# Kernel optimization log

Measured on AMD Instinct MI355X. Metric: run time of the kernel, lower is better.

The kernel has to match this reference:

```python
import jax, jax.numpy as jnp
import numpy as np

N = 50000      # nodes
E = 800000     # edges
FEAT = 128     # input feature dim
EMB = 256      # embed_dim = heads * hid
H = 4          # attention heads
C = 64         # hid_dim per head
PED = 32       # positional encoding dim
NEG_SLOPE = 0.2


def setup_inputs() -> dict:
    key = jax.random.key(0)
    ks = jax.random.split(key, 20)
    s = lambda i, shape, sc=0.1: jax.random.normal(ks[i], shape, jnp.float32) * sc
    return {
        "x": s(0, (N, FEAT), 1.0),
        "x_masked": s(1, (N, FEAT), 1.0),
        "PE": s(2, (N, PED), 1.0),
        "PE_noise": s(3, (N, PED), 1.0),
        "edge_index": jax.random.randint(ks[4], (2, E), 0, N),
        # PEG positional encoder (linear + relu)
        "W_peg": s(5, (PED, PED)), "b_peg": jnp.zeros((PED,), jnp.float32),
        # GAT layer 0
        "W0": s(6, (FEAT, H * C)), "a_s0": s(7, (H, C)), "a_d0": s(8, (H, C)),
        "w_pe0": s(9, (H,)), "W_u0": s(10, (PED, PED)),
        # GAT layer 1
        "W1": s(11, (EMB, H * C)), "a_s1": s(12, (H, C)), "a_d1": s(13, (H, C)),
        "w_pe1": s(14, (H,)), "W_u1": s(15, (PED, PED)),
    }


def _gat(x, pe, src, dst, W, a_s, a_d, w_pe, W_u):
    # PE-aware GATConv: standard GAT attention + PE-distance bias per head.
    xp = (x @ W).reshape(-1, H, C)                       # [N,H,C]
    al_s = (xp * a_s).sum(-1)                            # [N,H]
    al_d = (xp * a_d).sum(-1)                            # [N,H]
    dist = jnp.sqrt(((pe[src] - pe[dst]) ** 2).sum(-1) + 1e-8)   # [E]
    logits = jax.nn.leaky_relu(al_s[src] + al_d[dst], NEG_SLOPE) \
             + dist[:, None] * w_pe                      # [E,H]
    # segment softmax over incoming edges of each dst node
    m = jax.ops.segment_max(logits, dst, num_segments=N)
    e = jnp.exp(logits - m[dst])
    den = jax.ops.segment_sum(e, dst, num_segments=N)
    alpha = e / (den[dst] + 1e-16)                       # [E,H]
    out = jax.ops.segment_sum(alpha[:, :, None] * xp[src], dst,
                              num_segments=N).reshape(-1, H * C)  # [N,H*C]
    pe_out = jax.nn.relu(pe @ W_u)                       # per-layer PE update
    return out, pe_out


def reference(x, x_masked, PE, PE_noise, W_peg, b_peg,
              W0, a_s0, a_d0, w_pe0, W_u0,
              W1, a_s1, a_d1, w_pe1, W_u1, edge_index):
    src, dst = edge_index[0], edge_index[1]
    # PEG encoder on both PE branches
    pe = jax.nn.relu(PE @ W_peg + b_peg)
    pe_n = jax.nn.relu(PE_noise @ W_peg + b_peg)
    # layer 0 (dual branches; eval mode -> dropout is identity)
    h, pe_n = _gat(x, pe_n, src, dst, W0, a_s0, a_d0, w_pe0, W_u0)
    hm, pe = _gat(x_masked, pe, src, dst, W0, a_s0, a_d0, w_pe0, W_u0)
    h = jax.nn.relu(h)
    hm = jax.nn.relu(hm)
    # layer 1 (last layer: no activation)
    h, pe_n = _gat(h, pe_n, src, dst, W1, a_s1, a_d1, w_pe1, W_u1)
    hm, pe = _gat(hm, pe, src, dst, W1, a_s1, a_d1, w_pe1, W_u1)
    return (hm, pe_n)
```

## Files before the change

kernel.cpp:

```cpp
#include <hip/hip_runtime.h>
#include <hip/hip_bf16.h>

#define N_NODES 50000
#define N_EDGES 800000
#define NEG_SLOPE 0.2f

typedef __hip_bfloat16 bf16;
typedef __attribute__((ext_vector_type(8))) short short8;
typedef __attribute__((ext_vector_type(4))) float f32x4;
typedef __attribute__((ext_vector_type(2))) float f32x2;

__device__ __forceinline__ float b2f(bf16 x) { return __bfloat162float(x); }

__device__ __forceinline__ float ldsel(const void* p, size_t i, int isbf) {
  return isbf ? __bfloat162float(((const bf16*)p)[i]) : ((const float*)p)[i];
}
__device__ __forceinline__ void stsel(void* p, size_t i, int isbf, float v) {
  if (isbf) ((bf16*)p)[i] = __float2bfloat16(v);
  else ((float*)p)[i] = v;
}

__device__ __forceinline__ int block_detect(const unsigned short* __restrict__ probe) {
  __shared__ int wcount;
  int tid = threadIdx.x;
  if (tid == 0) wcount = 0;
  __syncthreads();
  int ex = (probe[2 * tid] >> 7) & 0xFF;
  unsigned long long m = __ballot(ex >= 0x85);
  if ((tid & 63) == 0) atomicAdd(&wcount, __popcll(m));
  __syncthreads();
  return wcount < 8;
}

struct CvtJobs {
  const void* src[10];
  float* dst[10];
  int n[10];
};
__global__ __launch_bounds__(256) void prep_kernel(CvtJobs jobs,
                                                   const unsigned short* __restrict__ probe,
                                                   const void* __restrict__ W0in,
                                                   bf16* __restrict__ Wt0,
                                                   const void* __restrict__ W1in,
                                                   bf16* __restrict__ Wt1,
                                                   int* __restrict__ flag,
                                                   const int* __restrict__ dst,
                                                   int* __restrict__ deg) {
  int tid = threadIdx.x;
  int b = blockIdx.x;
  if (b >= 400) {
    int e = (b - 400) * 256 + tid;
    atomicAdd(&deg[dst[e]], 1);
    return;
  }
  int isbf = block_detect(probe);
  if (b == 0 && tid == 0) *flag = isbf;
  if (b < 16) {
    for (int j = 0; j < 10; j++) {
      int n = jobs.n[j];
      const void* s = jobs.src[j];
      float* d = jobs.dst[j];
      for (int i = b * 256 + tid; i < n; i += 16 * 256) d[i] = ldsel(s, i, isbf);
    }
  } else if (b < 16 + 128) {
    int i = (b - 16) * 256 + tid;
    int n = i >> 7, k = i & 127;
    Wt0[i] = __float2bfloat16(ldsel(W0in, (size_t)k * 256 + n, isbf));
  } else {
    int i = (b - 144) * 256 + tid;
    int n = i >> 8, k = i & 255;
    Wt1[i] = __float2bfloat16(ldsel(W1in, (size_t)k * 256 + n, isbf));
  }
}

__global__ __launch_bounds__(1024) void scan_kernel(const int* __restrict__ deg,
                                                    int* __restrict__ rowptr,
                                                    int* __restrict__ bsum,
                                                    int* __restrict__ flags, int n) {
  __shared__ int wsum[16];
  __shared__ int spre;
  int tid = threadIdx.x;
  int idx = blockIdx.x * 1024 + tid;
  int v = (idx < n) ? deg[idx] : 0;
  int incl = v;
#pragma unroll
  for (int off = 1; off < 64; off <<= 1) {
    int t = __shfl_up(incl, off);
    if ((tid & 63) >= off) incl += t;
  }
  int wid = tid >> 6;
  if ((tid & 63) == 63) wsum[wid] = incl;
  __syncthreads();
  if (tid == 0) {
    int acc = 0;
#pragma unroll
    for (int w = 0; w < 16; w++) {
      int t = wsum[w];
      wsum[w] = acc;
      acc += t;
    }
    atomicExch(&bsum[blockIdx.x], acc);
    if (atomicAdd(&flags[0], 1) == 48) {
      int a = 0;
      for (int j = 0; j < 49; j++) {
        int t = atomicAdd(&bsum[j], 0);
        atomicExch(&bsum[j], a);
        a += t;
      }
      atomicExch(&flags[1], 1);
    }
    while (atomicAdd(&flags[1], 0) == 0) {}
    spre = atomicAdd(&bsum[blockIdx.x], 0);
  }
  __syncthreads();
  if (idx < n) rowptr[idx + 1] = spre + wsum[wid] + incl;
  if (idx == 0) rowptr[0] = 0;
}

template <int K, bool A_DUAL>
__device__ __forceinline__ void gemm_body(char* smem, int bid, int tid,
                                          const void* __restrict__ Ap,
                                          const bf16* __restrict__ Bt,
                                          bf16* __restrict__ C, int M,
                                          const float* __restrict__ a_sf,
                                          const float* __restrict__ a_df,
                                          char* __restrict__ blob,
                                          float* __restrict__ al_d,
                                          const int* __restrict__ flag) {
  constexpr int LDK = 72;
  short* a_lds = (short*)smem;
  short* b_lds = (short*)(smem + 64 * LDK * 2);
  float* lds_al = (float*)(smem + 2 * 64 * LDK * 2);
  int nrt = (M + 63) / 64;
  int xcd = bid & 7;
  int jj = bid >> 3;
  int col_t = jj & 3;
  int row_t = (jj >> 2) * 8 + xcd;
  if (row_t >= nrt) return;
  int isbf = A_DUAL ? *flag : 1;
  int row0 = row_t * 64;
  int col0 = col_t * 64;
  int lane = tid & 63;
  int wv = tid >> 6;
  int wm = (wv & 1) * 32, wn = (wv >> 1) * 32;
  int l15 = lane & 15, quad = lane >> 4;
  if (tid < 128) lds_al[tid] = 0.f;
  f32x4 acc00 = {0.f, 0.f, 0.f, 0.f}, acc01 = acc00, acc10 = acc00, acc11 = acc00;

  for (int kb = 0; kb < K; kb += 64) {
    if (kb) __syncthreads();
    for (int idx = tid; idx < 64 * 8; idx += 256) {
      int r = idx >> 3, sidx = idx & 7;
      int gr = row0 + r;
      size_t gi = (size_t)gr * K + kb + sidx * 8;
      uint4 av = make_uint4(0u, 0u, 0u, 0u);
      if (A_DUAL && !isbf) {
        if (gr < M) {
          float4 f0 = ((const float4*)Ap)[gi / 4];
          float4 f1 = ((const float4*)Ap)[gi / 4 + 1];
          union { uint4 v; bf16 h[8]; } o;
          o.h[0] = __float2bfloat16(f0.x);
          o.h[1] = __float2bfloat16(f0.y);
          o.h[2] = __float2bfloat16(f0.z);
          o.h[3] = __float2bfloat16(f0.w);
          o.h[4] = __float2bfloat16(f1.x);
          o.h[5] = __float2bfloat16(f1.y);
          o.h[6] = __float2bfloat16(f1.z);
          o.h[7] = __float2bfloat16(f1.w);
          av = o.v;
        }
      } else {
        if (gr < M) av = *(const uint4*)&((const bf16*)Ap)[gi];
      }
      *(uint4*)&a_lds[r * LDK + sidx * 8] = av;
      *(uint4*)&b_lds[r * LDK + sidx * 8] =
          *(const uint4*)&Bt[(size_t)(col0 + r) * K + kb + sidx * 8];
    }
    __syncthreads();
#pragma unroll
    for (int k0 = 0; k0 < 64; k0 += 32) {
      int ko = k0 + quad * 8;
      short8 a0 = *(const short8*)&a_lds[(wm + l15) * LDK + ko];
      short8 a1 = *(const short8*)&a_lds[(wm + 16 + l15) * LDK + ko];
      short8 b0 = *(const short8*)&b_lds[(wn + l15) * LDK + ko];
      short8 b1 = *(const short8*)&b_lds[(wn + 16 + l15) * LDK + ko];
      acc00 = __builtin_amdgcn_mfma_f32_16x16x32_bf16(a0, b0, acc00, 0, 0, 0);
      acc01 = __builtin_amdgcn_mfma_f32_16x16x32_bf16(a0, b1, acc01, 0, 0, 0);
      acc10 = __builtin_amdgcn_mfma_f32_16x16x32_bf16(a1, b0, acc10, 0, 0, 0);
      acc11 = __builtin_amdgcn_mfma_f32_16x16x32_bf16(a1, b1, acc11, 0, 0, 0);
    }
  }
  const f32x4* accs[2][2] = {{&acc00, &acc01}, {&acc10, &acc11}};
  float as0 = a_sf[col0 + wn + l15], as1 = a_sf[col0 + wn + 16 + l15];
  float ad0 = a_df[col0 + wn + l15], ad1 = a_df[col0 + wn + 16 + l15];
#pragma unroll
  for (int i = 0; i < 2; i++) {
    float sp[4], dp[4];
#pragma unroll
    for (int r = 0; r < 4; r++) {
      float v0 = (*accs[i][0])[r], v1 = (*accs[i][1])[r];
      sp[r] = v0 * as0 + v1 * as1;
      dp[r] = v0 * ad0 + v1 * ad1;
      int grow = row0 + wm + i * 16 + quad * 4 + r;
      if (grow < M) {
        C[(size_t)grow * 256 + col0 + wn + l15] = __float2bfloat16(v0);
        C[(size_t)grow * 256 + col0 + wn + 16 + l15] = __float2bfloat16(v1);
      }
    }
#pragma unroll
    for (int off = 1; off < 16; off <<= 1) {
#pragma unroll
      for (int r = 0; r < 4; r++) {
        sp[r] += __shfl_xor(sp[r], off);
        dp[r] += __shfl_xor(dp[r], off);
      }
    }
    if (l15 == 0) {
#pragma unroll
      for (int r = 0; r < 4; r++) {
        int lrow = wm + i * 16 + quad * 4 + r;
        atomicAdd(&lds_al[lrow], sp[r]);
        atomicAdd(&lds_al[64 + lrow], dp[r]);
      }
    }
  }
  __syncthreads();
  if (tid < 64 && row0 + tid < M) {
    int row = row0 + tid;
    *(float*)(blob + (size_t)row * 128 + 64 + (size_t)col_t * 4) = lds_al[tid];
    al_d[(size_t)row * 4 + col_t] = lds_al[64 + tid];
  }
}

#define SMEM_BYTES (2 * 64 * 72 * 2 + 512)

template <int K, bool A_DUAL>
__global__ __launch_bounds__(256) void mfma_gemm(const void* __restrict__ Ap,
                                                 const bf16* __restrict__ Bt,
                                                 bf16* __restrict__ C, int M,
                                                 const float* __restrict__ a_sf,
                                                 const float* __restrict__ a_df,
                                                 char* __restrict__ blob,
                                                 float* __restrict__ al_d,
                                                 const int* __restrict__ flag) {
  __shared__ char smem[SMEM_BYTES];
  gemm_body<K, A_DUAL>(smem, blockIdx.x, threadIdx.x, Ap, Bt, C, M, a_sf, a_df,
                       blob, al_d, flag);
}

#define NGEMM0 3136
#define NCHUNK (N_EDGES / 256)
#define NFILL8 (NCHUNK * 8)
#define NDIV8 (N_NODES / 8)
__global__ __launch_bounds__(256) void mid_kernel(const void* __restrict__ Ap,
                                                  const bf16* __restrict__ Wt0,
                                                  bf16* __restrict__ xp,
                                                  const float* __restrict__ a_s0,
                                                  const float* __restrict__ a_d0,
                                                  float* __restrict__ al_d,
                                                  const int* __restrict__ src,
                                                  const int* __restrict__ dst,
                                                  const int* __restrict__ rowptr,
                                                  int* __restrict__ fill,
                                                  int* __restrict__ csr_src,
                                                  const void* __restrict__ pen,
                                                  const void* __restrict__ pem,
                                                  const float* __restrict__ Wpeg,
                                                  const float* __restrict__ bpeg,
                                                  const float* __restrict__ Wu0,
                                                  const float* __restrict__ Wu1,
                                                  void* out, size_t out_off,
                                                  char* __restrict__ blob0,
                                                  char* __restrict__ blob1,
                                                  const int* __restrict__ flag) {
  __shared__ char smem[SMEM_BYTES];
  int tid = threadIdx.x;
  int b = blockIdx.x;
  if (b < NGEMM0) {
    gemm_body<128, true>(smem, b, tid, Ap, Wt0, xp, N_NODES, a_s0, a_d0, blob0,
                         al_d, flag);
    return;
  }
  b -= NGEMM0;
  if (b < NFILL8) {
    int xcd = b & 7;
    int e = (b >> 3) * 256 + tid;
    int d = dst[e];
    int lo = xcd * NDIV8;
    if (d >= lo && d < lo + NDIV8) {
      int pos = atomicAdd(&fill[d], 1);
      csr_src[rowptr[d] + pos] = src[e];
    }
    return;
  }
  int pb = b - NFILL8;
  float* w1 = (float*)smem;
  float* w2 = w1 + 1024;
  float* w3 = w2 + 1024;
  float* rowA = w3 + 1024;
  float* rowB = rowA + 256;
  int isbf = *flag;
  bool c3 = pb < NDIV8;
  int n0 = (c3 ? pb : pb - NDIV8) * 8;
  const void* in = c3 ? pen : pem;
  for (int i = tid; i < 1024; i += 256) {
    w1[i] = Wpeg[i];
    w2[i] = Wu0[i];
    if (c3) w3[i] = Wu1[i];
  }
  rowA[tid] = ldsel(in, (size_t)n0 * 32 + tid, isbf);
  __syncthreads();
  int col = tid & 31, ln = tid >> 5;
  size_t bi = ((size_t)(n0 + ln)) * 64 + col;
  float acc = bpeg[col];
#pragma unroll
  for (int j = 0; j < 32; j++) acc += rowA[ln * 32 + j] * w1[j * 32 + col];
  acc = fmaxf(acc, 0.f);
  if (!c3) ((bf16*)blob0)[bi] = __float2bfloat16(acc);
  rowB[tid] = acc;
  __syncthreads();
  acc = 0.f;
#pragma unroll
  for (int j = 0; j < 32; j++) acc += rowB[ln * 32 + j] * w2[j * 32 + col];
  acc = fmaxf(acc, 0.f);
  if (!c3) {
    ((bf16*)blob1)[bi] = __float2bfloat16(acc);
    return;
  }
  rowA[tid] = acc;
  __syncthreads();
  acc = 0.f;
#pragma unroll
  for (int j = 0; j < 32; j++) acc += rowA[ln * 32 + j] * w3[j * 32 + col];
  stsel(out, out_off + (size_t)n0 * 32 + tid, isbf, fmaxf(acc, 0.f));
}

template <bool RELU, bool OUT_DUAL>
__global__ __launch_bounds__(256) void agg_kernel(const bf16* __restrict__ xp,
                                                  const char* __restrict__ blob,
                                                  const float* __restrict__ al_d,
                                                  const float* __restrict__ w_pe,
                                                  const int* __restrict__ csr_src,
                                                  const int* __restrict__ rowptr,
                                                  void* out, const int* __restrict__ flag) {
  int isbf = OUT_DUAL ? *flag : 1;
  int lane = threadIdx.x & 63;
  int n = blockIdx.x * 4 + (threadIdx.x >> 6);
  int q = lane >> 4, li = lane & 15, h = li >> 2;
  const char* bn = blob + (size_t)n * 128;
  unsigned int ud = *(const unsigned int*)(bn + li * 4);
  float pdlo = __uint_as_float(ud << 16);
  float pdhi = __uint_as_float(ud & 0xffff0000u);
  float ald = al_d[(size_t)n * 4 + h];
  float wph = w_pe[h];
  int s1 = rowptr[n + 1];
  int s = rowptr[n] + q;
  f32x2 acc2[8];
#pragma unroll
  for (int j = 0; j < 8; j++) acc2[j] = (f32x2){0.f, 0.f};
  float asum = 0.f;

  int sn_c = -1, sn_n = -1;
  unsigned int pes_c = 0, pes_n = 0;
  float als_c = 0.f, als_n = 0.f;
  uint4 z = make_uint4(0u, 0u, 0u, 0u);
  uint4 xc0 = z, xc1 = z, xn0 = z, xn1 = z;
  if (s < s1) {
    sn_c = csr_src[s];
    const char* bs = blob + (size_t)sn_c * 128;
    pes_c = *(const unsigned int*)(bs + li * 4);
    als_c = *(const float*)(bs + 64 + h * 4);
    const uint4* b = (const uint4*)&xp[(size_t)sn_c * 256 + li * 16];
    xc0 = b[0];
    xc1 = b[1];
    if (s + 4 < s1) sn_n = csr_src[s + 4];
  }
  int sf = s + 8;
  while (sn_c >= 0) {
    if (sn_n >= 0) {
      const char* bs = blob + (size_t)sn_n * 128;
      pes_n = *(const unsigned int*)(bs + li * 4);
      als_n = *(const float*)(bs + 64 + h * 4);
      const uint4* b = (const uint4*)&xp[(size_t)sn_n * 256 + li * 16];
      xn0 = b[0];
      xn1 = b[1];
    }
    int sn_f = (sf < s1) ? csr_src[sf] : -1;
    sf += 4;
    float dx = __uint_as_float(pes_c << 16) - pdlo;
    float dy = __uint_as_float(pes_c & 0xffff0000u) - pdhi;
    float d2 = dx * dx + dy * dy;
#pragma unroll
    for (int off = 1; off < 16; off <<= 1) d2 += __shfl_xor(d2, off);
    float lg = als_c + ald;
    lg = fmaxf(lg, 0.f) + NEG_SLOPE * fminf(lg, 0.f);
    lg += __builtin_amdgcn_sqrtf(d2 + 1e-8f) * wph;
    float a = __expf(lg);
    f32x2 av = {a, a};
    unsigned int u[8] = {xc0.x, xc0.y, xc0.z, xc0.w, xc1.x, xc1.y, xc1.z, xc1.w};
#pragma unroll
    for (int p = 0; p < 8; p++) {
      f32x2 xv;
      xv.x = __uint_as_float(u[p] << 16);
      xv.y = __uint_as_float(u[p] & 0xffff0000u);
      acc2[p] += av * xv;
    }
    asum += a;
    sn_c = sn_n;
    pes_c = pes_n;
    als_c = als_n;
    xc0 = xn0;
    xc1 = xn1;
    sn_n = sn_f;
  }
#pragma unroll
  for (int j = 0; j < 8; j++) {
    acc2[j].x += __shfl_xor(acc2[j].x, 16);
    acc2[j].x += __shfl_xor(acc2[j].x, 32);
    acc2[j].y += __shfl_xor(acc2[j].y, 16);
    acc2[j].y += __shfl_xor(acc2[j].y, 32);
  }
  asum += __shfl_xor(asum, 16);
  asum += __shfl_xor(asum, 32);
  if (q == 0) {
    float inv = 1.f / (asum + 1e-16f);
    size_t oi = (size_t)n * 256 + li * 16;
    if (OUT_DUAL && !isbf) {
      float* of = (float*)out;
#pragma unroll
      for (int p = 0; p < 4; p++) {
        float4 f;
        f.x = acc2[2 * p].x * inv;
        f.y = acc2[2 * p].y * inv;
        f.z = acc2[2 * p + 1].x * inv;
        f.w = acc2[2 * p + 1].y * inv;
        if (RELU) {
          f.x = fmaxf(f.x, 0.f);
          f.y = fmaxf(f.y, 0.f);
          f.z = fmaxf(f.z, 0.f);
          f.w = fmaxf(f.w, 0.f);
        }
        *(float4*)&of[oi + 4 * p] = f;
      }
    } else {
      union { uint4 v[2]; bf16 hh[16]; } o;
#pragma unroll
      for (int j = 0; j < 8; j++) {
        float rlo = acc2[j].x * inv;
        float rhi = acc2[j].y * inv;
        if (RELU) {
          rlo = fmaxf(rlo, 0.f);
          rhi = fmaxf(rhi, 0.f);
        }
        o.hh[2 * j] = __float2bfloat16(rlo);
        o.hh[2 * j + 1] = __float2bfloat16(rhi);
      }
      uint4* ob = (uint4*)&((bf16*)out)[oi];
      ob[0] = o.v[0];
      ob[1] = o.v[1];
    }
  }
}

extern "C" void kernel_launch(void* const* d_in, const int* in_sizes, int n_in,
                              void* d_out, int out_size, void* d_ws, size_t ws_size,
                              hipStream_t stream) {
  const void* x_masked = d_in[1];
  const void* PE = d_in[2];
  const void* PE_noise = d_in[3];
  const int* ei = (const int*)d_in[4];
  const int* src = ei;
  const int* dst = ei + N_EDGES;

  char* w = (char*)d_ws;
  auto alloc = [&](size_t bytes) -> char* {
    char* p = w;
    w += (bytes + 255) / 256 * 256;
    return p;
  };
  int* flag = (int*)alloc(4);
  float* W_peg_f = (float*)alloc(1024 * 4);
  float* b_peg_f = (float*)alloc(32 * 4);
  float* a_s0_f = (float*)alloc(256 * 4);
  float* a_d0_f = (float*)alloc(256 * 4);
  float* w_pe0_f = (float*)alloc(4 * 4);
  float* W_u0_f = (float*)alloc(1024 * 4);
  float* a_s1_f = (float*)alloc(256 * 4);
  float* a_d1_f = (float*)alloc(256 * 4);
  float* w_pe1_f = (float*)alloc(4 * 4);
  float* W_u1_f = (float*)alloc(1024 * 4);
  bf16* Wt0 = (bf16*)alloc(32768 * 2);
  bf16* Wt1 = (bf16*)alloc(65536 * 2);
  char* blob0 = alloc((size_t)N_NODES * 128);
  char* blob1 = alloc((size_t)N_NODES * 128);
  float* al_d = (float*)alloc((size_t)N_NODES * 4 * 4);
  int* degfill = (int*)alloc(((size_t)N_NODES * 2 + 64) * 4);
  int* deg = degfill;
  int* fill = degfill + N_NODES;
  int* sflags = degfill + 2 * N_NODES;
  int* rowptr = (int*)alloc((size_t)(N_NODES + 1) * 4);
  int* bsum = (int*)alloc(64 * 4);
  int* csr_src = (int*)alloc((size_t)N_EDGES * 4);
  bf16* xp = (bf16*)alloc((size_t)N_NODES * 256 * 2);
  bf16* hm0 = (bf16*)alloc((size_t)N_NODES * 256 * 2);

  CvtJobs jobs;
  int ji = 0;
  auto addjob = [&](const void* s, float* d, int n) {
    jobs.src[ji] = s; jobs.dst[ji] = d; jobs.n[ji] = n; ji++;
  };
  addjob(d_in[5], W_peg_f, 1024);
  addjob(d_in[6], b_peg_f, 32);
  addjob(d_in[8], a_s0_f, 256);
  addjob(d_in[9], a_d0_f, 256);
  addjob(d_in[10], w_pe0_f, 4);
  addjob(d_in[11], W_u0_f, 1024);
  addjob(d_in[13], a_s1_f, 256);
  addjob(d_in[14], a_d1_f, 256);
  addjob(d_in[15], w_pe1_f, 4);
  addjob(d_in[16], W_u1_f, 1024);

  hipMemsetAsync(degfill, 0, ((size_t)N_NODES * 2 + 64) * 4, stream);

  prep_kernel<<<400 + NCHUNK, 256, 0, stream>>>(
      jobs, (const unsigned short*)d_in[5], d_in[7], Wt0, d_in[12], Wt1, flag,
      dst, deg);

  scan_kernel<<<49, 1024, 0, stream>>>(deg, rowptr, bsum, sflags, N_NODES);

  mid_kernel<<<NGEMM0 + NFILL8 + 2 * NDIV8, 256, 0, stream>>>(
      x_masked, Wt0, xp, a_s0_f, a_d0_f, al_d, src, dst, rowptr, fill, csr_src,
      PE_noise, PE, W_peg_f, b_peg_f, W_u0_f, W_u1_f, d_out,
      (size_t)N_NODES * 256, blob0, blob1, flag);

  agg_kernel<true, false><<<N_NODES / 4, 256, 0, stream>>>(
      xp, blob0, al_d, w_pe0_f, csr_src, rowptr, hm0, flag);

  mfma_gemm<256, false><<<NGEMM0, 256, 0, stream>>>(hm0, Wt1, xp, N_NODES,
                                                    a_s1_f, a_d1_f, blob1, al_d, flag);
  agg_kernel<false, true><<<N_NODES / 4, 256, 0, stream>>>(
      xp, blob1, al_d, w_pe1_f, csr_src, rowptr, d_out, flag);
}
```

Measured before the change: 447.4 us.

## Split GEMM out of fused mid kernel and widen GEMM K-tile to 128

The layer-0 GEMM is no longer packed into the same launch as the CSR fill and PE encoder work. The fill/PE blocks now run as their own kernel, and the GEMM becomes a standalone launch. The GEMM K-step doubles from 64 to 128, halving the number of LDS load/sync rounds at the cost of larger shared memory per block. This gives up the overlap of GEMM with fill/PE work inside one launch, and the larger LDS footprint may reduce occupancy.

```diff
diff --git a/kernel.cpp b/kernel.cpp
--- a/kernel.cpp
+++ b/kernel.cpp
@@ -117,27 +117,98 @@
   if (idx == 0) rowptr[0] = 0;
 }
 
+#define NCHUNK (N_EDGES / 256)
+#define NFILL8 (NCHUNK * 8)
+#define NDIV8 (N_NODES / 8)
+__global__ __launch_bounds__(256) void fill_peg_kernel(const int* __restrict__ src,
+                                                       const int* __restrict__ dst,
+                                                       const int* __restrict__ rowptr,
+                                                       int* __restrict__ fill,
+                                                       int* __restrict__ csr_src,
+                                                       const void* __restrict__ pen,
+                                                       const void* __restrict__ pem,
+                                                       const float* __restrict__ Wpeg,
+                                                       const float* __restrict__ bpeg,
+                                                       const float* __restrict__ Wu0,
+                                                       const float* __restrict__ Wu1,
+                                                       void* out, size_t out_off,
+                                                       char* __restrict__ blob0,
+                                                       char* __restrict__ blob1,
+                                                       const int* __restrict__ flag) {
+  __shared__ float w1[1024], w2[1024], w3[1024];
+  __shared__ float rowA[256], rowB[256];
+  int tid = threadIdx.x;
+  int b = blockIdx.x;
+  if (b < NFILL8) {
+    int xcd = b & 7;
+    int e = (b >> 3) * 256 + tid;
+    int d = dst[e];
+    int lo = xcd * NDIV8;
+    if (d >= lo && d < lo + NDIV8) {
+      int pos = atomicAdd(&fill[d], 1);
+      csr_src[rowptr[d] + pos] = src[e];
+    }
+    return;
+  }
+  int pb = b - NFILL8;
+  int isbf = *flag;
+  bool c3 = pb < NDIV8;
+  int n0 = (c3 ? pb : pb - NDIV8) * 8;
+  const void* in = c3 ? pen : pem;
+  for (int i = tid; i < 1024; i += 256) {
+    w1[i] = Wpeg[i];
+    w2[i] = Wu0[i];
+    if (c3) w3[i] = Wu1[i];
+  }
+  rowA[tid] = ldsel(in, (size_t)n0 * 32 + tid, isbf);
+  __syncthreads();
+  int col = tid & 31, ln = tid >> 5;
+  size_t bi = ((size_t)(n0 + ln)) * 64 + col;
+  float acc = bpeg[col];
+#pragma unroll
+  for (int j = 0; j < 32; j++) acc += rowA[ln * 32 + j] * w1[j * 32 + col];
+  acc = fmaxf(acc, 0.f);
+  if (!c3) ((bf16*)blob0)[bi] = __float2bfloat16(acc);
+  rowB[tid] = acc;
+  __syncthreads();
+  acc = 0.f;
+#pragma unroll
+  for (int j = 0; j < 32; j++) acc += rowB[ln * 32 + j] * w2[j * 32 + col];
+  acc = fmaxf(acc, 0.f);
+  if (!c3) {
+    ((bf16*)blob1)[bi] = __float2bfloat16(acc);
+    return;
+  }
+  rowA[tid] = acc;
+  __syncthreads();
+  acc = 0.f;
+#pragma unroll
+  for (int j = 0; j < 32; j++) acc += rowA[ln * 32 + j] * w3[j * 32 + col];
+  stsel(out, out_off + (size_t)n0 * 32 + tid, isbf, fmaxf(acc, 0.f));
+}
+
 template <int K, bool A_DUAL>
-__device__ __forceinline__ void gemm_body(char* smem, int bid, int tid,
-                                          const void* __restrict__ Ap,
-                                          const bf16* __restrict__ Bt,
-                                          bf16* __restrict__ C, int M,
-                                          const float* __restrict__ a_sf,
-                                          const float* __restrict__ a_df,
-                                          char* __restrict__ blob,
-                                          float* __restrict__ al_d,
-                                          const int* __restrict__ flag) {
-  constexpr int LDK = 72;
-  short* a_lds = (short*)smem;
-  short* b_lds = (short*)(smem + 64 * LDK * 2);
-  float* lds_al = (float*)(smem + 2 * 64 * LDK * 2);
+__global__ __launch_bounds__(256) void mfma_gemm(const void* __restrict__ Ap,
+                                                 const bf16* __restrict__ Bt,
+                                                 bf16* __restrict__ C, int M,
+                                                 const float* __restrict__ a_sf,
+                                                 const float* __restrict__ a_df,
+                                                 char* __restrict__ blob,
+                                                 float* __restrict__ al_d,
+                                                 const int* __restrict__ flag) {
+  constexpr int LDK = 136;
+  __shared__ short a_lds[64 * LDK];
+  __shared__ short b_lds[64 * LDK];
+  __shared__ float lds_al[128];
   int nrt = (M + 63) / 64;
+  int bid = blockIdx.x;
   int xcd = bid & 7;
   int jj = bid >> 3;
   int col_t = jj & 3;
   int row_t = (jj >> 2) * 8 + xcd;
   if (row_t >= nrt) return;
   int isbf = A_DUAL ? *flag : 1;
+  int tid = threadIdx.x;
   int row0 = row_t * 64;
   int col0 = col_t * 64;
   int lane = tid & 63;
@@ -147,10 +218,10 @@
   if (tid < 128) lds_al[tid] = 0.f;
   f32x4 acc00 = {0.f, 0.f, 0.f, 0.f}, acc01 = acc00, acc10 = acc00, acc11 = acc00;
 
-  for (int kb = 0; kb < K; kb += 64) {
+  for (int kb = 0; kb < K; kb += 128) {
     if (kb) __syncthreads();
-    for (int idx = tid; idx < 64 * 8; idx += 256) {
-      int r = idx >> 3, sidx = idx & 7;
+    for (int idx = tid; idx < 64 * 16; idx += 256) {
+      int r = idx >> 4, sidx = idx & 15;
       int gr = row0 + r;
       size_t gi = (size_t)gr * K + kb + sidx * 8;
       uint4 av = make_uint4(0u, 0u, 0u, 0u);
@@ -178,7 +249,7 @@
     }
     __syncthreads();
 #pragma unroll
-    for (int k0 = 0; k0 < 64; k0 += 32) {
+    for (int k0 = 0; k0 < 128; k0 += 32) {
       int ko = k0 + quad * 8;
       short8 a0 = *(const short8*)&a_lds[(wm + l15) * LDK + ko];
       short8 a1 = *(const short8*)&a_lds[(wm + 16 + l15) * LDK + ko];
@@ -230,109 +301,6 @@
     *(float*)(blob + (size_t)row * 128 + 64 + (size_t)col_t * 4) = lds_al[tid];
     al_d[(size_t)row * 4 + col_t] = lds_al[64 + tid];
   }
-}
-
-#define SMEM_BYTES (2 * 64 * 72 * 2 + 512)
-
-template <int K, bool A_DUAL>
-__global__ __launch_bounds__(256) void mfma_gemm(const void* __restrict__ Ap,
-                                                 const bf16* __restrict__ Bt,
-                                                 bf16* __restrict__ C, int M,
-                                                 const float* __restrict__ a_sf,
-                                                 const float* __restrict__ a_df,
-                                                 char* __restrict__ blob,
-                                                 float* __restrict__ al_d,
-                                                 const int* __restrict__ flag) {
-  __shared__ char smem[SMEM_BYTES];
-  gemm_body<K, A_DUAL>(smem, blockIdx.x, threadIdx.x, Ap, Bt, C, M, a_sf, a_df,
-                       blob, al_d, flag);
-}
-
-#define NGEMM0 3136
-#define NCHUNK (N_EDGES / 256)
-#define NFILL8 (NCHUNK * 8)
-#define NDIV8 (N_NODES / 8)
-__global__ __launch_bounds__(256) void mid_kernel(const void* __restrict__ Ap,
-                                                  const bf16* __restrict__ Wt0,
-                                                  bf16* __restrict__ xp,
-                                                  const float* __restrict__ a_s0,
-                                                  const float* __restrict__ a_d0,
-                                                  float* __restrict__ al_d,
-                                                  const int* __restrict__ src,
-                                                  const int* __restrict__ dst,
-                                                  const int* __restrict__ rowptr,
-                                                  int* __restrict__ fill,
-                                                  int* __restrict__ csr_src,
-                                                  const void* __restrict__ pen,
-                                                  const void* __restrict__ pem,
-                                                  const float* __restrict__ Wpeg,
-                                                  const float* __restrict__ bpeg,
-                                                  const float* __restrict__ Wu0,
-                                                  const float* __restrict__ Wu1,
-                                                  void* out, size_t out_off,
-                                                  char* __restrict__ blob0,
-                                                  char* __restrict__ blob1,
-                                                  const int* __restrict__ flag) {
-  __shared__ char smem[SMEM_BYTES];
-  int tid = threadIdx.x;
-  int b = blockIdx.x;
-  if (b < NGEMM0) {
-    gemm_body<128, true>(smem, b, tid, Ap, Wt0, xp, N_NODES, a_s0, a_d0, blob0,
-                         al_d, flag);
-    return;
-  }
-  b -= NGEMM0;
-  if (b < NFILL8) {
-    int xcd = b & 7;
-    int e = (b >> 3) * 256 + tid;
-    int d = dst[e];
-    int lo = xcd * NDIV8;
-    if (d >= lo && d < lo + NDIV8) {
-      int pos = atomicAdd(&fill[d], 1);
-      csr_src[rowptr[d] + pos] = src[e];
-    }
-    return;
-  }
-  int pb = b - NFILL8;
-  float* w1 = (float*)smem;
-  float* w2 = w1 + 1024;
-  float* w3 = w2 + 1024;
-  float* rowA = w3 + 1024;
-  float* rowB = rowA + 256;
-  int isbf = *flag;
-  bool c3 = pb < NDIV8;
-  int n0 = (c3 ? pb : pb - NDIV8) * 8;
-  const void* in = c3 ? pen : pem;
-  for (int i = tid; i < 1024; i += 256) {
-    w1[i] = Wpeg[i];
-    w2[i] = Wu0[i];
-    if (c3) w3[i] = Wu1[i];
-  }
-  rowA[tid] = ldsel(in, (size_t)n0 * 32 + tid, isbf);
-  __syncthreads();
-  int col = tid & 31, ln = tid >> 5;
-  size_t bi = ((size_t)(n0 + ln)) * 64 + col;
-  float acc = bpeg[col];
-#pragma unroll
-  for (int j = 0; j < 32; j++) acc += rowA[ln * 32 + j] * w1[j * 32 + col];
-  acc = fmaxf(acc, 0.f);
-  if (!c3) ((bf16*)blob0)[bi] = __float2bfloat16(acc);
-  rowB[tid] = acc;
-  __syncthreads();
-  acc = 0.f;
-#pragma unroll
-  for (int j = 0; j < 32; j++) acc += rowB[ln * 32 + j] * w2[j * 32 + col];
-  acc = fmaxf(acc, 0.f);
-  if (!c3) {
-    ((bf16*)blob1)[bi] = __float2bfloat16(acc);
-    return;
-  }
-  rowA[tid] = acc;
-  __syncthreads();
-  acc = 0.f;
-#pragma unroll
-  for (int j = 0; j < 32; j++) acc += rowA[ln * 32 + j] * w3[j * 32 + col];
-  stsel(out, out_off + (size_t)n0 * 32 + tid, isbf, fmaxf(acc, 0.f));
 }
 
 template <bool RELU, bool OUT_DUAL>
@@ -528,16 +496,20 @@
 
   scan_kernel<<<49, 1024, 0, stream>>>(deg, rowptr, bsum, sflags, N_NODES);
 
-  mid_kernel<<<NGEMM0 + NFILL8 + 2 * NDIV8, 256, 0, stream>>>(
-      x_masked, Wt0, xp, a_s0_f, a_d0_f, al_d, src, dst, rowptr, fill, csr_src,
-      PE_noise, PE, W_peg_f, b_peg_f, W_u0_f, W_u1_f, d_out,
-      (size_t)N_NODES * 256, blob0, blob1, flag);
-
+  fill_peg_kernel<<<NFILL8 + 2 * NDIV8, 256, 0, stream>>>(
+      src, dst, rowptr, fill, csr_src, PE_noise, PE, W_peg_f, b_peg_f, W_u0_f,
+      W_u1_f, d_out, (size_t)N_NODES * 256, blob0, blob1, flag);
+
+  int nrt = (N_NODES + 63) / 64;
+  int gblk = ((nrt + 7) / 8) * 8 * 4;
+
+  mfma_gemm<128, true><<<gblk, 256, 0, stream>>>(x_masked, Wt0, xp, N_NODES,
+                                                 a_s0_f, a_d0_f, blob0, al_d, flag);
   agg_kernel<true, false><<<N_NODES / 4, 256, 0, stream>>>(
       xp, blob0, al_d, w_pe0_f, csr_src, rowptr, hm0, flag);
 
-  mfma_gemm<256, false><<<NGEMM0, 256, 0, stream>>>(hm0, Wt1, xp, N_NODES,
-                                                    a_s1_f, a_d1_f, blob1, al_d, flag);
+  mfma_gemm<256, false><<<gblk, 256, 0, stream>>>(hm0, Wt1, xp, N_NODES,
+                                                  a_s1_f, a_d1_f, blob1, al_d, flag);
   agg_kernel<false, true><<<N_NODES / 4, 256, 0, stream>>>(
       xp, blob1, al_d, w_pe1_f, csr_src, rowptr, d_out, flag);
 }
```

After: 453.4 us. Within noise of the previous version (+1.4%).
